# Performance work log

Hardware: AMD Instinct MI355X
Metric: run time of the kernel (lower is better)

The kernel has to match this reference:

```python
import jax, jax.numpy as jnp
import numpy as np

# ---- module hyperparameters (init_kwargs) ----
V0 = 1.0
SIGMA0 = 0.5
GAUSS_CONST = V0 / (np.sqrt(2.0 * np.pi) * SIGMA0)
NW, NF, D, H = 4096, 16, 3, 256  # walkers, fermions, dimensions, hidden width
N = NF * D


def setup_inputs() -> dict:
    key = jax.random.key(0)
    k0, k1, k2, k3 = jax.random.split(key, 4)
    sc = lambda k, shape, fan_in: jax.random.normal(k, shape, jnp.float32) / np.sqrt(fan_in).astype(np.float32)
    return {
        "x": jax.random.normal(k0, (NW, NF, D), jnp.float32),
        "W1": sc(k1, (N, H), N),
        "b1": jnp.zeros((H,), jnp.float32),
        "W2": sc(k2, (H, H), H),
        "b2": jnp.zeros((H,), jnp.float32),
        "w3": sc(k3, (H,), H),
        "b3": jnp.zeros((), jnp.float32),
    }


def _logpsi(xf, W1, b1, W2, b2, w3, b3):
    # xf: (N,) flattened single-walker coordinates -> scalar log|psi|
    h = jnp.tanh(xf @ W1 + b1)
    h = jnp.tanh(h @ W2 + b2)
    return h @ w3 + b3


def reference(x, W1, b1, W2, b2, w3, b3):
    nw, nf, d = x.shape
    xflat = x.reshape(nw, nf * d)

    f = lambda xf: _logpsi(xf, W1, b1, W2, b2, w3, b3)
    grad_f = jax.grad(f)

    def kinetic_one(xf):
        g = grad_f(xf)                      # (N,) d logpsi / dx
        hess = jax.jacfwd(grad_f)(xf)       # (N, N) forward-over-reverse Hessian
        lap = jnp.trace(hess)
        return -0.5 * (lap + jnp.sum(g * g))

    kin = jax.vmap(kinetic_one)(xflat)      # (nw,)

    # harmonic potential 1/2 sum x^2
    pot = 0.5 * jnp.sum(xflat * xflat, axis=1)

    # Gaussian interaction, faithful to source: unsqueeze(-2)/unsqueeze(-1) on
    # (nw, nf, d) broadcasts to (nw, nf, d, d) intra-particle coordinate diffs,
    # then sum over last axis -> (nw, nf, d), triu(k=1) over trailing (nf, d).
    diff = x[..., None, :] - x[..., :, None]            # (nw, nf, d, d)
    sqdist = jnp.sum(diff * diff, axis=-1)              # (nw, nf, d)
    mask = jnp.triu(jnp.ones((nf, d), x.dtype), k=1)    # (nf, d)
    inter = GAUSS_CONST * jnp.sum(jnp.exp(-sqdist / (2.0 * SIGMA0 ** 2)) * mask, axis=(-2, -1))

    eloc = kin + pot + inter
    return (eloc, kin, pot, inter)
```

## Files before the change

### kernel.cpp

```cpp
#include <hip/hip_runtime.h>
#include <cmath>

#define NWALK 4096
#define NXD   48
#define HID   256
#define WPB   8
#define GCONST 0.7978845608028654f

typedef _Float16 half8   __attribute__((ext_vector_type(8)));
typedef float    float4v __attribute__((ext_vector_type(4)));

__global__ __launch_bounds__(256) void prep_all(const float* __restrict__ W2,
                                                const float* __restrict__ W1,
                                                const float* __restrict__ x,
                                                const float* __restrict__ b1,
                                                _Float16* __restrict__ W2c,
                                                _Float16* __restrict__ W1c,
                                                _Float16* __restrict__ t1h,
                                                _Float16* __restrict__ h1h,
                                                _Float16* __restrict__ ch) {
    __shared__ float tile[64][65];
    __shared__ float xs[16][NXD];

    if (blockIdx.x < 16) {
        const int bi = blockIdx.x & 3;
        const int bj = blockIdx.x >> 2;
        const int tx = threadIdx.x & 63;
        const int ty = threadIdx.x >> 6;
        #pragma unroll
        for (int r = 0; r < 16; ++r) {
            int il = ty * 16 + r;
            tile[tx][il] = W2[(bi * 64 + il) * HID + bj * 64 + tx];
        }
        __syncthreads();
        #pragma unroll
        for (int r = 0; r < 16; ++r) {
            int jl = ty * 16 + r;
            W2c[(bj * 64 + jl) * HID + bi * 64 + tx] = (_Float16)tile[jl][tx];
        }
        #pragma unroll
        for (int r = 0; r < 3; ++r) {
            int k = blockIdx.x * 3 + r;
            W1c[k * HID + threadIdx.x] = (_Float16)W1[k * HID + threadIdx.x];
        }
    } else {
        const int i  = threadIdx.x;
        const int w0 = (blockIdx.x - 16) * 16;

        float col[NXD];
        float S = 0.f;
        #pragma unroll
        for (int k = 0; k < NXD; ++k) {
            float v = W1[k * HID + i];
            col[k] = v;
            S = fmaf(v, v, S);
        }
        #pragma unroll
        for (int t = threadIdx.x; t < 16 * NXD; t += 256)
            ((float*)xs)[t] = x[w0 * NXD + t];
        __syncthreads();

        const float b = b1[i];
        #pragma unroll 4
        for (int w = 0; w < 16; ++w) {
            float a1 = b;
            #pragma unroll
            for (int k = 0; k < NXD; ++k)
                a1 = fmaf(xs[w][k], col[k], a1);
            float h1 = tanhf(a1);
            float t1 = 1.f - h1 * h1;
            int off = (w0 + w) * HID + i;
            t1h[off] = (_Float16)t1;
            h1h[off] = (_Float16)h1;
            ch[off]  = (_Float16)(S * h1 * t1);
        }
    }
}

__global__ __launch_bounds__(256, 2) void eloc8(
    const float* __restrict__ x,
    const float* __restrict__ b2,
    const float* __restrict__ w3,
    const _Float16* __restrict__ W2c,
    const _Float16* __restrict__ W1c,
    const _Float16* __restrict__ t1h,
    const _Float16* __restrict__ h1h,
    const _Float16* __restrict__ ch,
    float* __restrict__ out)
{
    __shared__ __align__(16) _Float16 AsT[2][50 * HID];
    __shared__ float xs[WPB][NXD];
    __shared__ float b2s[HID], w3s[HID];
    __shared__ float a2s[HID], ps[HID], us[HID], uh2s[HID];
    __shared__ float gw[2][4][NXD];
    __shared__ float wred[2][4][2];

    const int w0   = blockIdx.x * WPB;
    const int tid  = threadIdx.x;
    const int wave = tid >> 6;
    const int lane = tid & 63;
    const int n16  = lane & 15;
    const int quad = (tid >> 4) & 3;
    const int ci   = tid & 31;
    const int k0   = tid >> 5;

    half8 afr[8][4];
    #pragma unroll
    for (int s = 0; s < 8; ++s)
        #pragma unroll
        for (int a = 0; a < 4; ++a)
            afr[s][a] = *(const half8*)(W2c + ((wave * 4 + a) * 16 + n16) * HID
                                        + s * 32 + quad * 8);

    b2s[tid] = b2[tid];
    w3s[tid] = w3[tid];
    #pragma unroll
    for (int t = tid; t < WPB * NXD; t += 256)
        ((float*)xs)[t] = x[w0 * NXD + t];

    {
        half8 th = *(const half8*)(t1h + w0 * HID + ci * 8);
        #pragma unroll
        for (int s2 = 0; s2 < 6; ++s2) {
            int k = s2 * 8 + k0;
            half8 wv = *(const half8*)(W1c + k * HID + ci * 8);
            *(half8*)(AsT[0] + k * HID + ((ci ^ (k & 7)) * 8)) = wv * th;
        }
        if (tid < 32) {
            half8 hv = *(const half8*)(h1h + w0 * HID + tid * 8);
            *(half8*)(AsT[0] + 48 * HID + tid * 8) = hv;
        } else if (tid < 64) {
            int c2 = tid - 32;
            half8 cv = *(const half8*)(ch + w0 * HID + c2 * 8);
            *(half8*)(AsT[0] + 49 * HID + ((c2 ^ 1) * 8)) = cv;
        }
    }
    __syncthreads();

    for (int ww = 0; ww < WPB; ++ww) {
        const int cur = ww & 1, nxt = cur ^ 1;
        const int wg  = w0 + ww;
        const _Float16* curA = AsT[cur];
        const bool more = (ww + 1 < WPB);

        {
            float4v acc[4];
            #pragma unroll
            for (int a = 0; a < 4; ++a) acc[a] = (float4v){0.f, 0.f, 0.f, 0.f};
            const int krow = 48 + (n16 & 1);
            #pragma unroll
            for (int s = 0; s < 8; ++s) {
                half8 bf = *(const half8*)(curA + krow * HID
                            + ((((s * 4 + quad) ^ (krow & 7)) << 3)));
                #pragma unroll
                for (int a = 0; a < 4; ++a)
                    acc[a] = __builtin_amdgcn_mfma_f32_16x16x32_f16(
                        afr[s][a], bf, acc[a], 0, 0, 0);
            }
            if (n16 == 0) {
                #pragma unroll
                for (int a = 0; a < 4; ++a)
                    #pragma unroll
                    for (int reg = 0; reg < 4; ++reg)
                        a2s[(wave * 4 + a) * 16 + quad * 4 + reg] = acc[a][reg];
            } else if (n16 == 1) {
                #pragma unroll
                for (int a = 0; a < 4; ++a)
                    #pragma unroll
                    for (int reg = 0; reg < 4; ++reg)
                        ps[(wave * 4 + a) * 16 + quad * 4 + reg] = acc[a][reg];
            }
        }

        float a2v = a2s[tid] + b2s[tid];
        float h2  = tanhf(a2v);
        float t2  = 1.f - h2 * h2;
        float u   = w3s[tid] * t2;
        us[tid]   = u;
        uh2s[tid] = u * h2;
        float rt2 = u * ps[tid];

        float uu_r[4][4], uh_r[4][4];
        #pragma unroll
        for (int a = 0; a < 4; ++a)
            #pragma unroll
            for (int reg = 0; reg < 4; ++reg) {
                int j = (wave * 4 + a) * 16 + quad * 4 + reg;
                uu_r[a][reg] = us[j];
                uh_r[a][reg] = uh2s[j];
            }

        float rt1 = 0.f;
        float gp[3];
        #pragma unroll 1
        for (int kt = 0; kt < 3; ++kt) {
            float4v acc[4];
            #pragma unroll
            for (int a = 0; a < 4; ++a) acc[a] = (float4v){0.f, 0.f, 0.f, 0.f};
            const int krow = kt * 16 + n16;
            #pragma unroll
            for (int s = 0; s < 8; ++s) {
                half8 bf = *(const half8*)(curA + krow * HID
                            + ((((s * 4 + quad) ^ (krow & 7)) << 3)));
                #pragma unroll
                for (int a = 0; a < 4; ++a)
                    acc[a] = __builtin_amdgcn_mfma_f32_16x16x32_f16(
                        afr[s][a], bf, acc[a], 0, 0, 0);
            }
            float g = 0.f;
            #pragma unroll
            for (int a = 0; a < 4; ++a)
                #pragma unroll
                for (int reg = 0; reg < 4; ++reg) {
                    float m = acc[a][reg];
                    rt1 = fmaf(m * m, uh_r[a][reg], rt1);
                    g   = fmaf(m, uu_r[a][reg], g);
                }
            gp[kt] = g;
        }

        if (more) {
            const int wn = wg + 1;
            half8 th = *(const half8*)(t1h + wn * HID + ci * 8);
            #pragma unroll
            for (int s2 = 0; s2 < 6; ++s2) {
                int k = s2 * 8 + k0;
                half8 wv = *(const half8*)(W1c + k * HID + ci * 8);
                *(half8*)(AsT[nxt] + k * HID + ((ci ^ (k & 7)) * 8)) = wv * th;
            }
            if (tid < 32) {
                half8 hv = *(const half8*)(h1h + wn * HID + tid * 8);
                *(half8*)(AsT[nxt] + 48 * HID + tid * 8) = hv;
            } else if (tid < 64) {
                half8 cv = *(const half8*)(ch + wn * HID + (tid - 32) * 8);
                *(half8*)(AsT[nxt] + 49 * HID + (((tid - 32) ^ 1) * 8)) = cv;
            }
        }

        #pragma unroll
        for (int off = 32; off > 0; off >>= 1) {
            rt1 += __shfl_down(rt1, off, 64);
            rt2 += __shfl_down(rt2, off, 64);
        }
        #pragma unroll
        for (int kt = 0; kt < 3; ++kt) {
            gp[kt] += __shfl_xor(gp[kt], 16, 64);
            gp[kt] += __shfl_xor(gp[kt], 32, 64);
        }
        if (lane == 0) { wred[cur][wave][0] = rt1; wred[cur][wave][1] = rt2; }
        if (lane < 16) {
            #pragma unroll
            for (int kt = 0; kt < 3; ++kt) gw[cur][wave][kt * 16 + lane] = gp[kt];
        }

        __syncthreads();

        if (wave == 0) {
            float ggp = 0.f, potp = 0.f;
            if (lane < NXD) {
                float g = gw[cur][0][lane] + gw[cur][1][lane]
                        + gw[cur][2][lane] + gw[cur][3][lane];
                ggp = g * g;
                float xq = xs[ww][lane];
                potp = 0.5f * xq * xq;
            }
            #pragma unroll
            for (int off = 32; off > 0; off >>= 1) {
                ggp  += __shfl_down(ggp, off, 64);
                potp += __shfl_down(potp, off, 64);
            }
            if (lane == 0) {
                float T1 = wred[cur][0][0] + wred[cur][1][0] + wred[cur][2][0] + wred[cur][3][0];
                float T2 = wred[cur][0][1] + wred[cur][1][1] + wred[cur][2][1] + wred[cur][3][1];
                float kin = T1 + T2 - 0.5f * ggp;

                float x0 = xs[ww][0], x1 = xs[ww][1], x2 = xs[ww][2];
                float x3 = xs[ww][3], x4 = xs[ww][4], x5 = xs[ww][5];
                float d01 = (x0-x1)*(x0-x1) + (x2-x1)*(x2-x1);
                float d02 = (x0-x2)*(x0-x2) + (x1-x2)*(x1-x2);
                float d12 = (x3-x5)*(x3-x5) + (x4-x5)*(x4-x5);
                float inter = GCONST * (expf(-2.f*d01) + expf(-2.f*d02) + expf(-2.f*d12));

                out[wg]             = kin + potp + inter;
                out[NWALK + wg]     = kin;
                out[2 * NWALK + wg] = potp;
                out[3 * NWALK + wg] = inter;
            }
        }
    }
}

extern "C" void kernel_launch(void* const* d_in, const int* in_sizes, int n_in,
                              void* d_out, int out_size, void* d_ws, size_t ws_size,
                              hipStream_t stream) {
    const float* x  = (const float*)d_in[0];
    const float* W1 = (const float*)d_in[1];
    const float* b1 = (const float*)d_in[2];
    const float* W2 = (const float*)d_in[3];
    const float* b2 = (const float*)d_in[4];
    const float* w3 = (const float*)d_in[5];
    float* out = (float*)d_out;

    char* ws = (char*)d_ws;
    _Float16* W2c = (_Float16*)(ws);
    _Float16* W1c = (_Float16*)(ws + 131072);
    _Float16* t1h = (_Float16*)(ws + 155648);
    _Float16* h1h = (_Float16*)(ws + 2252800);
    _Float16* chv = (_Float16*)(ws + 4349952);

    prep_all<<<16 + NWALK / 16, 256, 0, stream>>>(W2, W1, x, b1, W2c, W1c, t1h, h1h, chv);
    eloc8<<<NWALK / WPB, 256, 0, stream>>>(x, b2, w3, W2c, W1c, t1h, h1h, chv, out);
}
```

Measured before the change: 120.3 us.

## Split eloc8 across 8 waves and keep W1 fragments in registers

The eloc8 block grows from 256 to 512 threads. Each wave now owns 32 of the 256 hidden rows instead of 64, which halves the per-wave A-fragment registers and MFMA chains. The W1 tile is loaded once into registers and reused when building every walker's A matrix, and the next walker's inputs are prefetched earlier and written before the Hessian MFMA loop. The aim is more latency hiding and less redundant global traffic per walker, at the cost of more barrier participants, a larger cross-wave reduction, and idle lanes in the tanh stage.

```diff
diff --git a/kernel.cpp b/kernel.cpp
--- a/kernel.cpp
+++ b/kernel.cpp
@@ -77,7 +77,7 @@
     }
 }
 
-__global__ __launch_bounds__(256, 2) void eloc8(
+__global__ __launch_bounds__(512, 4) void eloc8(
     const float* __restrict__ x,
     const float* __restrict__ b2,
     const float* __restrict__ w3,
@@ -92,39 +92,40 @@
     __shared__ float xs[WPB][NXD];
     __shared__ float b2s[HID], w3s[HID];
     __shared__ float a2s[HID], ps[HID], us[HID], uh2s[HID];
-    __shared__ float gw[2][4][NXD];
-    __shared__ float wred[2][4][2];
+    __shared__ float gw[2][8][NXD];
+    __shared__ float wred[2][8][2];
 
     const int w0   = blockIdx.x * WPB;
     const int tid  = threadIdx.x;
     const int wave = tid >> 6;
     const int lane = tid & 63;
     const int n16  = lane & 15;
-    const int quad = (tid >> 4) & 3;
+    const int quad = lane >> 4;
     const int ci   = tid & 31;
-    const int k0   = tid >> 5;
-
-    half8 afr[8][4];
+    const int kr0  = (tid >> 5) & 15;
+
+    half8 afr[8][2];
     #pragma unroll
     for (int s = 0; s < 8; ++s)
         #pragma unroll
-        for (int a = 0; a < 4; ++a)
-            afr[s][a] = *(const half8*)(W2c + ((wave * 4 + a) * 16 + n16) * HID
+        for (int a = 0; a < 2; ++a)
+            afr[s][a] = *(const half8*)(W2c + ((wave * 2 + a) * 16 + n16) * HID
                                         + s * 32 + quad * 8);
 
-    b2s[tid] = b2[tid];
-    w3s[tid] = w3[tid];
+    half8 w1r[3];
     #pragma unroll
-    for (int t = tid; t < WPB * NXD; t += 256)
-        ((float*)xs)[t] = x[w0 * NXD + t];
+    for (int s2 = 0; s2 < 3; ++s2)
+        w1r[s2] = *(const half8*)(W1c + (s2 * 16 + kr0) * HID + ci * 8);
+
+    if (tid < HID) { b2s[tid] = b2[tid]; w3s[tid] = w3[tid]; }
+    if (tid < WPB * NXD) ((float*)xs)[tid] = x[w0 * NXD + tid];
 
     {
         half8 th = *(const half8*)(t1h + w0 * HID + ci * 8);
         #pragma unroll
-        for (int s2 = 0; s2 < 6; ++s2) {
-            int k = s2 * 8 + k0;
-            half8 wv = *(const half8*)(W1c + k * HID + ci * 8);
-            *(half8*)(AsT[0] + k * HID + ((ci ^ (k & 7)) * 8)) = wv * th;
+        for (int s2 = 0; s2 < 3; ++s2) {
+            int k = s2 * 16 + kr0;
+            *(half8*)(AsT[0] + k * HID + ((ci ^ (k & 7)) * 8)) = w1r[s2] * th;
         }
         if (tid < 32) {
             half8 hv = *(const half8*)(h1h + w0 * HID + tid * 8);
@@ -143,73 +144,90 @@
         const _Float16* curA = AsT[cur];
         const bool more = (ww + 1 < WPB);
 
+        float4v acc3[2];
+        acc3[0] = (float4v){0.f, 0.f, 0.f, 0.f};
+        acc3[1] = (float4v){0.f, 0.f, 0.f, 0.f};
         {
-            float4v acc[4];
-            #pragma unroll
-            for (int a = 0; a < 4; ++a) acc[a] = (float4v){0.f, 0.f, 0.f, 0.f};
             const int krow = 48 + (n16 & 1);
             #pragma unroll
             for (int s = 0; s < 8; ++s) {
                 half8 bf = *(const half8*)(curA + krow * HID
                             + ((((s * 4 + quad) ^ (krow & 7)) << 3)));
-                #pragma unroll
-                for (int a = 0; a < 4; ++a)
-                    acc[a] = __builtin_amdgcn_mfma_f32_16x16x32_f16(
-                        afr[s][a], bf, acc[a], 0, 0, 0);
-            }
-            if (n16 == 0) {
-                #pragma unroll
-                for (int a = 0; a < 4; ++a)
-                    #pragma unroll
-                    for (int reg = 0; reg < 4; ++reg)
-                        a2s[(wave * 4 + a) * 16 + quad * 4 + reg] = acc[a][reg];
-            } else if (n16 == 1) {
-                #pragma unroll
-                for (int a = 0; a < 4; ++a)
-                    #pragma unroll
-                    for (int reg = 0; reg < 4; ++reg)
-                        ps[(wave * 4 + a) * 16 + quad * 4 + reg] = acc[a][reg];
-            }
-        }
-
-        float a2v = a2s[tid] + b2s[tid];
-        float h2  = tanhf(a2v);
-        float t2  = 1.f - h2 * h2;
-        float u   = w3s[tid] * t2;
-        us[tid]   = u;
-        uh2s[tid] = u * h2;
-        float rt2 = u * ps[tid];
-
-        float uu_r[4][4], uh_r[4][4];
-        #pragma unroll
-        for (int a = 0; a < 4; ++a)
-            #pragma unroll
-            for (int reg = 0; reg < 4; ++reg) {
-                int j = (wave * 4 + a) * 16 + quad * 4 + reg;
-                uu_r[a][reg] = us[j];
-                uh_r[a][reg] = uh2s[j];
-            }
+                acc3[0] = __builtin_amdgcn_mfma_f32_16x16x32_f16(afr[s][0], bf, acc3[0], 0, 0, 0);
+                acc3[1] = __builtin_amdgcn_mfma_f32_16x16x32_f16(afr[s][1], bf, acc3[1], 0, 0, 0);
+            }
+        }
+
+        half8 th, hcv;
+        if (more) {
+            const int wn = wg + 1;
+            th = *(const half8*)(t1h + wn * HID + ci * 8);
+            if (tid < 32)      hcv = *(const half8*)(h1h + wn * HID + tid * 8);
+            else if (tid < 64) hcv = *(const half8*)(ch + wn * HID + (tid - 32) * 8);
+        }
+
+        if (n16 == 0) {
+            #pragma unroll
+            for (int a = 0; a < 2; ++a)
+                #pragma unroll
+                for (int reg = 0; reg < 4; ++reg)
+                    a2s[(wave * 2 + a) * 16 + quad * 4 + reg] = acc3[a][reg];
+        } else if (n16 == 1) {
+            #pragma unroll
+            for (int a = 0; a < 2; ++a)
+                #pragma unroll
+                for (int reg = 0; reg < 4; ++reg)
+                    ps[(wave * 2 + a) * 16 + quad * 4 + reg] = acc3[a][reg];
+        }
+
+        float rt2 = 0.f;
+        if (lane < 32) {
+            int j2 = wave * 32 + lane;
+            float a2v = a2s[j2] + b2s[j2];
+            float h2  = tanhf(a2v);
+            float t2  = 1.f - h2 * h2;
+            float u   = w3s[j2] * t2;
+            us[j2]    = u;
+            uh2s[j2]  = u * h2;
+            rt2 = u * ps[j2];
+        }
+
+        float4v uu_r[2], uh_r[2];
+        #pragma unroll
+        for (int a = 0; a < 2; ++a) {
+            int j0 = (wave * 2 + a) * 16 + quad * 4;
+            uu_r[a] = *(const float4v*)(us + j0);
+            uh_r[a] = *(const float4v*)(uh2s + j0);
+        }
+
+        if (more) {
+            #pragma unroll
+            for (int s2 = 0; s2 < 3; ++s2) {
+                int k = s2 * 16 + kr0;
+                *(half8*)(AsT[nxt] + k * HID + ((ci ^ (k & 7)) * 8)) = w1r[s2] * th;
+            }
+            if (tid < 32)      *(half8*)(AsT[nxt] + 48 * HID + tid * 8) = hcv;
+            else if (tid < 64) *(half8*)(AsT[nxt] + 49 * HID + (((tid - 32) ^ 1) * 8)) = hcv;
+        }
 
         float rt1 = 0.f;
         float gp[3];
         #pragma unroll 1
         for (int kt = 0; kt < 3; ++kt) {
-            float4v acc[4];
-            #pragma unroll
-            for (int a = 0; a < 4; ++a) acc[a] = (float4v){0.f, 0.f, 0.f, 0.f};
+            float4v acc[2];
+            acc[0] = (float4v){0.f, 0.f, 0.f, 0.f};
+            acc[1] = (float4v){0.f, 0.f, 0.f, 0.f};
             const int krow = kt * 16 + n16;
             #pragma unroll
             for (int s = 0; s < 8; ++s) {
                 half8 bf = *(const half8*)(curA + krow * HID
                             + ((((s * 4 + quad) ^ (krow & 7)) << 3)));
-                #pragma unroll
-                for (int a = 0; a < 4; ++a)
-                    acc[a] = __builtin_amdgcn_mfma_f32_16x16x32_f16(
-                        afr[s][a], bf, acc[a], 0, 0, 0);
+                acc[0] = __builtin_amdgcn_mfma_f32_16x16x32_f16(afr[s][0], bf, acc[0], 0, 0, 0);
+                acc[1] = __builtin_amdgcn_mfma_f32_16x16x32_f16(afr[s][1], bf, acc[1], 0, 0, 0);
             }
             float g = 0.f;
             #pragma unroll
-            for (int a = 0; a < 4; ++a)
+            for (int a = 0; a < 2; ++a)
                 #pragma unroll
                 for (int reg = 0; reg < 4; ++reg) {
                     float m = acc[a][reg];
@@ -219,24 +237,6 @@
             gp[kt] = g;
         }
 
-        if (more) {
-            const int wn = wg + 1;
-            half8 th = *(const half8*)(t1h + wn * HID + ci * 8);
-            #pragma unroll
-            for (int s2 = 0; s2 < 6; ++s2) {
-                int k = s2 * 8 + k0;
-                half8 wv = *(const half8*)(W1c + k * HID + ci * 8);
-                *(half8*)(AsT[nxt] + k * HID + ((ci ^ (k & 7)) * 8)) = wv * th;
-            }
-            if (tid < 32) {
-                half8 hv = *(const half8*)(h1h + wn * HID + tid * 8);
-                *(half8*)(AsT[nxt] + 48 * HID + tid * 8) = hv;
-            } else if (tid < 64) {
-                half8 cv = *(const half8*)(ch + wn * HID + (tid - 32) * 8);
-                *(half8*)(AsT[nxt] + 49 * HID + (((tid - 32) ^ 1) * 8)) = cv;
-            }
-        }
-
         #pragma unroll
         for (int off = 32; off > 0; off >>= 1) {
             rt1 += __shfl_down(rt1, off, 64);
@@ -258,8 +258,9 @@
         if (wave == 0) {
             float ggp = 0.f, potp = 0.f;
             if (lane < NXD) {
-                float g = gw[cur][0][lane] + gw[cur][1][lane]
-                        + gw[cur][2][lane] + gw[cur][3][lane];
+                float g = 0.f;
+                #pragma unroll
+                for (int v = 0; v < 8; ++v) g += gw[cur][v][lane];
                 ggp = g * g;
                 float xq = xs[ww][lane];
                 potp = 0.5f * xq * xq;
@@ -270,8 +271,9 @@
                 potp += __shfl_down(potp, off, 64);
             }
             if (lane == 0) {
-                float T1 = wred[cur][0][0] + wred[cur][1][0] + wred[cur][2][0] + wred[cur][3][0];
-                float T2 = wred[cur][0][1] + wred[cur][1][1] + wred[cur][2][1] + wred[cur][3][1];
+                float T1 = 0.f, T2 = 0.f;
+                #pragma unroll
+                for (int v = 0; v < 8; ++v) { T1 += wred[cur][v][0]; T2 += wred[cur][v][1]; }
                 float kin = T1 + T2 - 0.5f * ggp;
 
                 float x0 = xs[ww][0], x1 = xs[ww][1], x2 = xs[ww][2];
@@ -309,5 +311,5 @@
     _Float16* chv = (_Float16*)(ws + 4349952);
 
     prep_all<<<16 + NWALK / 16, 256, 0, stream>>>(W2, W1, x, b1, W2c, W1c, t1h, h1h, chv);
-    eloc8<<<NWALK / WPB, 256, 0, stream>>>(x, b2, w3, W2c, W1c, t1h, h1h, chv, out);
+    eloc8<<<NWALK / WPB, 512, 0, stream>>>(x, b2, w3, W2c, W1c, t1h, h1h, chv, out);
 }
```

New measurement: 179.0 us. 48.7% more time.

## Fuse first-layer forward into main kernel, keep activations in LDS

Applied to the files above, without the earlier changes.

Moves the first-layer matvec, tanh, and derivative computation from the prep kernel into the main eloc8 kernel. Each block computes t1, h1 and the curvature term for its 8 walkers straight into shared memory, so the fp16 intermediate arrays are no longer written to and re-read from global memory. The prep kernel shrinks to the 16 weight-conversion blocks. The change also vectorises the us/uh2s register loads as float4 and rotates which wave does the final per-walker reduction. In exchange it adds about 12 KB of shared memory per block, which may reduce occupancy, and each block redoes a fp32 48x256 W1 read.

```diff
diff --git a/kernel.cpp b/kernel.cpp
--- a/kernel.cpp
+++ b/kernel.cpp
@@ -10,85 +10,47 @@
 typedef _Float16 half8   __attribute__((ext_vector_type(8)));
 typedef float    float4v __attribute__((ext_vector_type(4)));
 
-__global__ __launch_bounds__(256) void prep_all(const float* __restrict__ W2,
-                                                const float* __restrict__ W1,
-                                                const float* __restrict__ x,
-                                                const float* __restrict__ b1,
-                                                _Float16* __restrict__ W2c,
-                                                _Float16* __restrict__ W1c,
-                                                _Float16* __restrict__ t1h,
-                                                _Float16* __restrict__ h1h,
-                                                _Float16* __restrict__ ch) {
+__global__ __launch_bounds__(256) void prep_w(const float* __restrict__ W2,
+                                              const float* __restrict__ W1,
+                                              _Float16* __restrict__ W2c,
+                                              _Float16* __restrict__ W1c) {
     __shared__ float tile[64][65];
-    __shared__ float xs[16][NXD];
-
-    if (blockIdx.x < 16) {
-        const int bi = blockIdx.x & 3;
-        const int bj = blockIdx.x >> 2;
-        const int tx = threadIdx.x & 63;
-        const int ty = threadIdx.x >> 6;
-        #pragma unroll
-        for (int r = 0; r < 16; ++r) {
-            int il = ty * 16 + r;
-            tile[tx][il] = W2[(bi * 64 + il) * HID + bj * 64 + tx];
-        }
-        __syncthreads();
-        #pragma unroll
-        for (int r = 0; r < 16; ++r) {
-            int jl = ty * 16 + r;
-            W2c[(bj * 64 + jl) * HID + bi * 64 + tx] = (_Float16)tile[jl][tx];
-        }
-        #pragma unroll
-        for (int r = 0; r < 3; ++r) {
-            int k = blockIdx.x * 3 + r;
-            W1c[k * HID + threadIdx.x] = (_Float16)W1[k * HID + threadIdx.x];
-        }
-    } else {
-        const int i  = threadIdx.x;
-        const int w0 = (blockIdx.x - 16) * 16;
-
-        float col[NXD];
-        float S = 0.f;
-        #pragma unroll
-        for (int k = 0; k < NXD; ++k) {
-            float v = W1[k * HID + i];
-            col[k] = v;
-            S = fmaf(v, v, S);
-        }
-        #pragma unroll
-        for (int t = threadIdx.x; t < 16 * NXD; t += 256)
-            ((float*)xs)[t] = x[w0 * NXD + t];
-        __syncthreads();
-
-        const float b = b1[i];
-        #pragma unroll 4
-        for (int w = 0; w < 16; ++w) {
-            float a1 = b;
-            #pragma unroll
-            for (int k = 0; k < NXD; ++k)
-                a1 = fmaf(xs[w][k], col[k], a1);
-            float h1 = tanhf(a1);
-            float t1 = 1.f - h1 * h1;
-            int off = (w0 + w) * HID + i;
-            t1h[off] = (_Float16)t1;
-            h1h[off] = (_Float16)h1;
-            ch[off]  = (_Float16)(S * h1 * t1);
-        }
+    const int bi = blockIdx.x & 3;
+    const int bj = blockIdx.x >> 2;
+    const int tx = threadIdx.x & 63;
+    const int ty = threadIdx.x >> 6;
+    #pragma unroll
+    for (int r = 0; r < 16; ++r) {
+        int il = ty * 16 + r;
+        tile[tx][il] = W2[(bi * 64 + il) * HID + bj * 64 + tx];
+    }
+    __syncthreads();
+    #pragma unroll
+    for (int r = 0; r < 16; ++r) {
+        int jl = ty * 16 + r;
+        W2c[(bj * 64 + jl) * HID + bi * 64 + tx] = (_Float16)tile[jl][tx];
+    }
+    #pragma unroll
+    for (int r = 0; r < 3; ++r) {
+        int k = blockIdx.x * 3 + r;
+        W1c[k * HID + threadIdx.x] = (_Float16)W1[k * HID + threadIdx.x];
     }
 }
 
 __global__ __launch_bounds__(256, 2) void eloc8(
     const float* __restrict__ x,
+    const float* __restrict__ W1,
+    const float* __restrict__ b1,
     const float* __restrict__ b2,
     const float* __restrict__ w3,
     const _Float16* __restrict__ W2c,
     const _Float16* __restrict__ W1c,
-    const _Float16* __restrict__ t1h,
-    const _Float16* __restrict__ h1h,
-    const _Float16* __restrict__ ch,
     float* __restrict__ out)
 {
     __shared__ __align__(16) _Float16 AsT[2][50 * HID];
+    __shared__ __align__(16) _Float16 t1L[WPB][HID];
+    __shared__ __align__(16) _Float16 h1L[WPB][HID];
+    __shared__ __align__(16) _Float16 cL[WPB][HID];
     __shared__ float xs[WPB][NXD];
     __shared__ float b2s[HID], w3s[HID];
     __shared__ float a2s[HID], ps[HID], us[HID], uh2s[HID];
@@ -117,9 +79,35 @@
     #pragma unroll
     for (int t = tid; t < WPB * NXD; t += 256)
         ((float*)xs)[t] = x[w0 * NXD + t];
+    __syncthreads();
 
     {
-        half8 th = *(const half8*)(t1h + w0 * HID + ci * 8);
+        const int i = tid;
+        float a1[WPB];
+        #pragma unroll
+        for (int w = 0; w < WPB; ++w) a1[w] = b1[i];
+        float S = 0.f;
+        #pragma unroll
+        for (int k = 0; k < NXD; ++k) {
+            float v = W1[k * HID + i];
+            S = fmaf(v, v, S);
+            #pragma unroll
+            for (int w = 0; w < WPB; ++w)
+                a1[w] = fmaf(xs[w][k], v, a1[w]);
+        }
+        #pragma unroll
+        for (int w = 0; w < WPB; ++w) {
+            float h1 = tanhf(a1[w]);
+            float t1 = 1.f - h1 * h1;
+            t1L[w][i] = (_Float16)t1;
+            h1L[w][i] = (_Float16)h1;
+            cL[w][i]  = (_Float16)(S * h1 * t1);
+        }
+    }
+    __syncthreads();
+
+    {
+        half8 th = *(const half8*)(&t1L[0][ci * 8]);
         #pragma unroll
         for (int s2 = 0; s2 < 6; ++s2) {
             int k = s2 * 8 + k0;
@@ -127,11 +115,11 @@
             *(half8*)(AsT[0] + k * HID + ((ci ^ (k & 7)) * 8)) = wv * th;
         }
         if (tid < 32) {
-            half8 hv = *(const half8*)(h1h + w0 * HID + tid * 8);
+            half8 hv = *(const half8*)(&h1L[0][tid * 8]);
             *(half8*)(AsT[0] + 48 * HID + tid * 8) = hv;
         } else if (tid < 64) {
             int c2 = tid - 32;
-            half8 cv = *(const half8*)(ch + w0 * HID + c2 * 8);
+            half8 cv = *(const half8*)(&cL[0][c2 * 8]);
             *(half8*)(AsT[0] + 49 * HID + ((c2 ^ 1) * 8)) = cv;
         }
     }
@@ -180,15 +168,13 @@
         uh2s[tid] = u * h2;
         float rt2 = u * ps[tid];
 
-        float uu_r[4][4], uh_r[4][4];
-        #pragma unroll
-        for (int a = 0; a < 4; ++a)
-            #pragma unroll
-            for (int reg = 0; reg < 4; ++reg) {
-                int j = (wave * 4 + a) * 16 + quad * 4 + reg;
-                uu_r[a][reg] = us[j];
-                uh_r[a][reg] = uh2s[j];
-            }
+        float4v uu_r[4], uh_r[4];
+        #pragma unroll
+        for (int a = 0; a < 4; ++a) {
+            int j0 = (wave * 4 + a) * 16 + quad * 4;
+            uu_r[a] = *(const float4v*)(us + j0);
+            uh_r[a] = *(const float4v*)(uh2s + j0);
+        }
 
         float rt1 = 0.f;
         float gp[3];
@@ -220,8 +206,8 @@
         }
 
         if (more) {
-            const int wn = wg + 1;
-            half8 th = *(const half8*)(t1h + wn * HID + ci * 8);
+            const int wn = ww + 1;
+            half8 th = *(const half8*)(&t1L[wn][ci * 8]);
             #pragma unroll
             for (int s2 = 0; s2 < 6; ++s2) {
                 int k = s2 * 8 + k0;
@@ -229,10 +215,10 @@
                 *(half8*)(AsT[nxt] + k * HID + ((ci ^ (k & 7)) * 8)) = wv * th;
             }
             if (tid < 32) {
-                half8 hv = *(const half8*)(h1h + wn * HID + tid * 8);
+                half8 hv = *(const half8*)(&h1L[wn][tid * 8]);
                 *(half8*)(AsT[nxt] + 48 * HID + tid * 8) = hv;
             } else if (tid < 64) {
-                half8 cv = *(const half8*)(ch + wn * HID + (tid - 32) * 8);
+                half8 cv = *(const half8*)(&cL[wn][(tid - 32) * 8]);
                 *(half8*)(AsT[nxt] + 49 * HID + (((tid - 32) ^ 1) * 8)) = cv;
             }
         }
@@ -255,7 +241,7 @@
 
         __syncthreads();
 
-        if (wave == 0) {
+        if (wave == (ww & 3)) {
             float ggp = 0.f, potp = 0.f;
             if (lane < NXD) {
                 float g = gw[cur][0][lane] + gw[cur][1][lane]
@@ -304,10 +290,7 @@
     char* ws = (char*)d_ws;
     _Float16* W2c = (_Float16*)(ws);
     _Float16* W1c = (_Float16*)(ws + 131072);
-    _Float16* t1h = (_Float16*)(ws + 155648);
-    _Float16* h1h = (_Float16*)(ws + 2252800);
-    _Float16* chv = (_Float16*)(ws + 4349952);
-
-    prep_all<<<16 + NWALK / 16, 256, 0, stream>>>(W2, W1, x, b1, W2c, W1c, t1h, h1h, chv);
-    eloc8<<<NWALK / WPB, 256, 0, stream>>>(x, b2, w3, W2c, W1c, t1h, h1h, chv, out);
+
+    prep_w<<<16, 256, 0, stream>>>(W2, W1, W2c, W1c);
+    eloc8<<<NWALK / WPB, 256, 0, stream>>>(x, W1, b1, b2, w3, W2c, W1c, out);
 }
```

Result: slower. 175.8 us (+46.1%).
